# Performance work log

Hardware: AMD Instinct MI355X
Metric: run time of the kernel (lower is better)

## Reference

```python
import math
import jax, jax.numpy as jnp
import numpy as np

B, N, L, E, D = 8, 4096, 256, 64, 128
Q4 = D // 4

def setup_inputs():
    key = jax.random.key(0)
    ks = jax.random.split(key, 24)
    s = 0.05
    return {
        "x_L": jax.random.normal(ks[0], (B, N), jnp.float32),
        "x_y_mask": (jax.random.uniform(ks[1], (B, N)) < 0.7).astype(jnp.float32),
        "y_mask_L": (jax.random.uniform(ks[2], (B, N)) < 0.3).astype(jnp.float32),
        "x_y_mark": jax.random.normal(ks[3], (B, L, 1), jnp.float32),
        "variable_indices": jax.random.randint(ks[4], (B, N), 0, E, jnp.int32),
        "time_indices": jax.random.randint(ks[5], (B, N), 0, L, jnp.int32),
        "N_OBS_MAX": N,
        "W_obs": jax.random.normal(ks[6], (2, D)) * s,
        "b_obs": jnp.zeros((D,), jnp.float32),
        "W_temp": jax.random.normal(ks[7], (1, D)) * s,
        "b_temp": jnp.zeros((D,), jnp.float32),
        "var_he_w": jax.random.normal(ks[8], (E, D), jnp.float32),
        "Wq": jax.random.normal(ks[9], (D, D)) * s,
        "bq": jnp.zeros((D,), jnp.float32),
        "Wk": jax.random.normal(ks[10], (D, D)) * s,
        "bk": jnp.zeros((D,), jnp.float32),
        "Wv": jax.random.normal(ks[11], (D, D)) * s,
        "bv": jnp.zeros((D,), jnp.float32),
        "threshold": jnp.float32(0.0),
        "merge_coef": jnp.float32(0.5),
        "Pr_w": jax.random.normal(ks[12], (3 * D, Q4)) * s,
        "Pr_b": jnp.zeros((Q4,), jnp.float32),
        "Pi_w": jax.random.normal(ks[13], (D, Q4)) * s,
        "Pi_b": jnp.zeros((Q4,), jnp.float32),
        "Pj_w": jax.random.normal(ks[14], (D, Q4)) * s,
        "Pj_b": jnp.zeros((Q4,), jnp.float32),
        "Pk_w": jax.random.normal(ks[15], (D, Q4)) * s,
        "Pk_b": jnp.zeros((Q4,), jnp.float32),
        "Qr": jnp.eye(Q4, dtype=jnp.float32) + jax.random.normal(ks[16], (Q4, Q4)) * s,
        "Qi": jax.random.normal(ks[17], (Q4, Q4)) * s,
        "Qj": jax.random.normal(ks[18], (Q4, Q4)) * s,
        "Qk": jax.random.normal(ks[19], (Q4, Q4)) * s,
        "fusion_bias": jnp.zeros((D,), jnp.float32),
    }

def reference(x_L, x_y_mask, y_mask_L, x_y_mark, variable_indices, time_indices,
              N_OBS_MAX, W_obs, b_obs, W_temp, b_temp, var_he_w,
              Wq, bq, Wk, bk, Wv, bv, threshold, merge_coef,
              Pr_w, Pr_b, Pi_w, Pi_b, Pj_w, Pj_b, Pk_w, Pk_b,
              Qr, Qi, Qj, Qk, fusion_bias):
    dt = x_L.dtype
    # --- HypergraphEncoder ---
    x2 = jnp.stack([x_L, 1.0 - x_y_mask + y_mask_L], axis=-1)          # (B,N,2)
    # temporal incidence: node n belongs to time hyperedge time_indices[n]
    t_inc = (time_indices[:, None, :] == jnp.arange(L)[None, :, None]).astype(dt)
    t_inc = t_inc * x_y_mask[:, None, :]                                # (B,L,N)
    v_inc = (jnp.arange(E)[None, :, None] == variable_indices[:, None, :]).astype(dt)
    v_inc = v_inc * x_y_mask[:, None, :]                                # (B,E,N)
    obs = jax.nn.relu(x2 @ W_obs + b_obs) * x_y_mask[..., None]         # (B,N,D)
    t_he = jnp.sin(x_y_mark @ W_temp + b_temp)                          # (B,L,D)
    v_he = jax.nn.relu(jnp.broadcast_to(var_he_w, (x_L.shape[0], E, D)))  # (B,E,D)
    # --- IrregularityAwareAttention over variable hyperedges ---
    q = v_he @ Wq + bq
    k = v_he @ Wk + bk
    v = v_he @ Wv + bv
    scores = jnp.einsum('bed,bfd->bef', q, k) / math.sqrt(D)            # (B,E,E)
    aux = jnp.einsum('ben,bfn->bef', v_inc, v_inc) / math.sqrt(v_inc.shape[-1])
    m = (aux != 0) & (scores > threshold)
    scores = jnp.where(m, (1.0 - merge_coef) * scores + merge_coef * aux, scores)
    attn = jax.nn.softmax(scores, axis=-1)
    v_he_att = jnp.einsum('bef,bfd->bed', attn, v)                      # (B,E,D)
    # --- gather hyperedge features to nodes via incidence ---
    tg = jnp.einsum('bln,bld->bnd', t_inc, t_he)                        # (B,N,D)
    vg = jnp.einsum('ben,bed->bnd', v_inc, v_he_att)                    # (B,N,D)
    # --- QuaternionStructuredFusion ---
    r = jnp.concatenate([obs, tg, vg], axis=-1) @ Pr_w + Pr_b           # (B,N,D/4)
    i = obs @ Pi_w + Pi_b
    j = tg @ Pj_w + Pj_b
    kq = vg @ Pk_w + Pk_b
    q_in = jnp.concatenate([r, i, j, kq], axis=-1)                      # (B,N,D)
    W = jnp.concatenate([
        jnp.concatenate([Qr, -Qi, -Qj, -Qk], axis=1),
        jnp.concatenate([Qi,  Qr, -Qk,  Qj], axis=1),
        jnp.concatenate([Qj,  Qk,  Qr, -Qi], axis=1),
        jnp.concatenate([Qk, -Qj,  Qi,  Qr], axis=1)], axis=0)          # (D,D)
    return q_in @ W.T + fusion_bias                                     # (B,N,D)
```

## Files before the change

### kernel.cpp

```cpp
#include <hip/hip_runtime.h>
#include <hip/hip_bf16.h>

#define B_ 8
#define N_ 4096
#define L_ 256
#define E_ 64
#define D_ 128

typedef const float* fp;
typedef __attribute__((ext_vector_type(8))) short short8;
typedef __attribute__((ext_vector_type(4))) float f32x4;

__device__ __forceinline__ short f2bf(float x) {
  __hip_bfloat16 h = __float2bfloat16(x);
  return __builtin_bit_cast(short, h);
}

__device__ __constant__ int   selT[16] = {0,1,2,3, 1,0,3,2, 2,3,0,1, 3,2,1,0};
__device__ __constant__ float sgnT[16] = {1.f,-1.f,-1.f,-1.f, 1.f,1.f,-1.f,1.f,
                                          1.f,1.f,1.f,-1.f, 1.f,-1.f,1.f,1.f};


__global__ __launch_bounds__(256) void k_setup(
    fp Pr_w, fp Pi_w, fp Pj_w, fp Pk_w,
    fp Pr_b, fp Pi_b, fp Pj_b, fp Pk_b,
    fp Qr, fp Qi, fp Qj, fp Qk, fp fusion_bias,
    fp var_he_w, fp Wq, fp bq, fp Wk, fp bk, fp Wv, fp bv,
    fp xmask, const int* vidx,
    float* ws) {
  int bid = blockIdx.x, tid = threadIdx.x;
  float* M = ws;
  unsigned short* m0frag = (unsigned short*)ws;
  float* c = ws + 49152;
  float* qkv = ws + 49280;
  float* cnt = ws + 73856;
  if (bid < 96) {
    __shared__ float qlds[4][32][33];
    {
      fp Qsrc[4] = {Qr, Qi, Qj, Qk};
      for (int lid = tid; lid < 4096; lid += 256) {
        int mat = lid >> 10, el = lid & 1023;
        qlds[mat][el >> 5][el & 31] = Qsrc[mat][el];
      }
    }
    __syncthreads();
    int m = bid >> 5, di0 = (bid & 31) * 4;
    int sub = tid >> 7, dd = tid & 127;
    int br = dd >> 5, a = dd & 31;
    const float* w0 = qlds[br][a];
    int t1 = br * 4 + m + 1;
    const float* w1 = qlds[selT[t1]][a];
    float s1 = sgnT[t1];
    fp Pm = (m == 0) ? Pi_w : (m == 1) ? Pj_w : Pk_w;
#pragma unroll
    for (int ii = 0; ii < 2; ++ii) {
      int di = di0 + ii * 2 + sub;
      const float* pr = Pr_w + (m * 128 + di) * 32;
      const float* pm = Pm + di * 32;
      float acc = 0.f;
#pragma unroll
      for (int q = 0; q < 32; ++q)
        acc += pr[q] * w0[q] + s1 * pm[q] * w1[q];
      if (m == 0) {
        int fn = dd >> 4, ft = di >> 5, hi = (di >> 3) & 3, j = di & 7;
        int l = hi * 16 + (dd & 15);
        m0frag[((fn * 4 + ft) * 64 + l) * 8 + j] = (unsigned short)f2bf(acc);
      } else {
        M[m * 16384 + di * 128 + dd] = acc;
      }
    }
    if (bid == 0 && tid < 128) {
      float acc = fusion_bias ? fusion_bias[tid] : 0.f;
#pragma unroll
      for (int bc = 0; bc < 4; ++bc) {
        fp Pb = (bc == 0) ? Pr_b : (bc == 1) ? Pi_b : (bc == 2) ? Pj_b : Pk_b;
        int t = br * 4 + bc;
        const float* wr = qlds[selT[t]][a];
        float sg = sgnT[t];
        float part = 0.f;
#pragma unroll
        for (int q = 0; q < 32; ++q) part += Pb[q] * wr[q];
        acc += sg * part;
      }
      c[tid] = acc;
    }
  } else if (bid < 192) {
    int id = (bid - 96) * 256 + tid;
    int which = id >> 13, rem = id & 8191, e = rem >> 7, d = rem & 127;
    fp W = (which == 0) ? Wq : (which == 1) ? Wk : Wv;
    fp bb = (which == 0) ? bq : (which == 1) ? bk : bv;
    float acc = bb[d];
    for (int d2 = 0; d2 < 128; ++d2)
      acc += fmaxf(var_he_w[e * 128 + d2], 0.f) * W[d2 * 128 + d];
    qkv[id] = acc;
  } else {
    __shared__ int hc[64];
    int b = bid - 192;
    if (tid < 64) hc[tid] = 0;
    __syncthreads();
    for (int n = tid; n < N_; n += 256)
      if (xmask[b * N_ + n] != 0.f)
        atomicAdd(&hc[vidx[b * N_ + n] & 63], 1);
    __syncthreads();
    if (tid < 64) cnt[b * 64 + tid] = (float)hc[tid];
  }
}

__global__ __launch_bounds__(128) void k_mid(
    fp thr_p, fp mc_p, fp mark, fp W_temp, fp b_temp,
    float* ws) {
  const float* M1 = ws + 16384;
  const float* M2 = ws + 32768;
  const float* qkv = ws + 49280;
  const float* cnt = ws + 73856;
  float* VG = ws + 74368;
  float* TG = ws + 139904;
  int bid = blockIdx.x, t = threadIdx.x;
  if (bid < 512) {
    __shared__ float buf[128];
    __shared__ float attn_s[64];
    int b = bid >> 6, e = bid & 63;
    const float* q = qkv;
    const float* k = qkv + 8192;
    const float* v = qkv + 16384;
    int f = t & 63, h = t >> 6;
    float part = 0.f;
    for (int d = h * 64; d < h * 64 + 64; ++d)
      part += q[e * 128 + d] * k[f * 128 + d];
    buf[t] = part;
    __syncthreads();
    if (t < 64) {
      float s = (buf[t] + buf[t + 64]) * 0.08838834764831845f;
      if (t == e) {
        float aux = cnt[b * 64 + e] * (1.f / 64.f);
        float thv = thr_p ? thr_p[0] : 0.f;
        float mc = mc_p ? mc_p[0] : 0.5f;
        if (aux != 0.f && s > thv) s = (1.f - mc) * s + mc * aux;
      }
      float m = s;
      for (int o = 32; o; o >>= 1) m = fmaxf(m, __shfl_xor(m, o));
      float ex = __expf(s - m);
      float sum = ex;
      for (int o = 32; o; o >>= 1) sum += __shfl_xor(sum, o);
      attn_s[t] = ex / sum;
    }
    __syncthreads();
    float va = 0.f;
    for (int ff = 0; ff < 64; ++ff) va += attn_s[ff] * v[ff * 128 + t];
    __syncthreads();
    buf[t] = va;
    __syncthreads();
    float acc = 0.f;
    for (int di = 0; di < 128; ++di) acc += buf[di] * M2[di * 128 + t];
    VG[(b * 64 + e) * 128 + t] = acc;
  } else {
    __shared__ float tb[4][128];
    int r0 = (bid - 512) * 4;
#pragma unroll
    for (int r = 0; r < 4; ++r)
      tb[r][t] = sinf(mark[r0 + r] * W_temp[t] + b_temp[t]);
    __syncthreads();
    float a0 = 0.f, a1 = 0.f, a2 = 0.f, a3 = 0.f;
    for (int di = 0; di < 128; ++di) {
      float m1v = M1[di * 128 + t];
      a0 += tb[0][di] * m1v;
      a1 += tb[1][di] * m1v;
      a2 += tb[2][di] * m1v;
      a3 += tb[3][di] * m1v;
    }
    TG[(r0 + 0) * 128 + t] = a0;
    TG[(r0 + 1) * 128 + t] = a1;
    TG[(r0 + 2) * 128 + t] = a2;
    TG[(r0 + 3) * 128 + t] = a3;
  }
}

__global__ __launch_bounds__(256) void k_mainf(
    fp x_L, fp x_y_mask, fp y_mask_L, const int* vidx, const int* tidx,
    fp W_obs, fp b_obs, const float* ws, float* out) {
  __shared__ short8 m0s[2048];
  const short8* fr = (const short8*)ws;
  const float* c = ws + 49152;
  const float* VG = ws + 74368;
  const float* TG = ws + 139904;
  int tid = threadIdx.x;
#pragma unroll
  for (int i = 0; i < 8; ++i) m0s[tid + i * 256] = fr[tid + i * 256];
  __syncthreads();

  int w = tid >> 6, l = tid & 63;
  int nb = blockIdx.x * 64 + w * 16;
  int b = blockIdx.x >> 6;

  int nodeA = nb + (l & 15);
  float mask = x_y_mask[nodeA];
  float xa = x_L[nodeA];
  float xb = 1.f - mask + y_mask_L[nodeA];
  short8 af[4];
#pragma unroll
  for (int ft = 0; ft < 4; ++ft) {
#pragma unroll
    for (int j = 0; j < 8; ++j) {
      int col = ft * 32 + ((l >> 4) << 3) + j;
      float o = fmaxf(xa * W_obs[col] + xb * W_obs[128 + col] + b_obs[col], 0.f) * mask;
      af[ft][j] = f2bf(o);
    }
  }

  f32x4 acc[8];
#pragma unroll
  for (int fn = 0; fn < 8; ++fn) acc[fn] = (f32x4)(0.f);
#pragma unroll
  for (int fn = 0; fn < 8; ++fn) {
#pragma unroll
    for (int ft = 0; ft < 4; ++ft) {
      short8 bf = m0s[(fn * 4 + ft) * 64 + l];
      acc[fn] = __builtin_amdgcn_mfma_f32_16x16x32_bf16(af[ft], bf, acc[fn], 0, 0, 0);
    }
  }

  int colbase = l & 15;
  float cv[8];
#pragma unroll
  for (int fn = 0; fn < 8; ++fn) cv[fn] = c[fn * 16 + colbase];
#pragma unroll
  for (int rg = 0; rg < 4; ++rg) {
    int node = nb + ((l >> 4) << 2) + rg;
    float m2 = x_y_mask[node];
    int ti = tidx[node] & 255, vi = vidx[node] & 63;
    const float* tgr = TG + (b * 256 + ti) * 128;
    const float* vgr = VG + (b * 64 + vi) * 128;
    float* orow = out + node * 128;
#pragma unroll
    for (int fn = 0; fn < 8; ++fn) {
      int col = fn * 16 + colbase;
      orow[col] = acc[fn][rg] + cv[fn] + m2 * (tgr[col] + vgr[col]);
    }
  }
}

extern "C" void kernel_launch(void* const* d_in, const int* in_sizes, int n_in,
                              void* d_out, int out_size, void* d_ws, size_t ws_size,
                              hipStream_t stream) {
  const void* P[33];
  {
    int p = 0;
    for (int i = 0; i < 33; ++i) {
      bool isopt = (i == 6 || i == 18 || i == 19);
      if (isopt) {
        if (p < n_in && in_sizes[p] == 1) P[i] = d_in[p++];
        else P[i] = nullptr;
      } else {
        P[i] = (p < n_in) ? d_in[p++] : nullptr;
      }
    }
  }
  fp x_L      = (fp)P[0];
  fp x_y_mask = (fp)P[1];
  fp y_mask_L = (fp)P[2];
  fp x_y_mark = (fp)P[3];
  const int* vidx = (const int*)P[4];
  const int* tidx = (const int*)P[5];
  fp W_obs = (fp)P[7];
  fp b_obs = (fp)P[8];
  fp W_temp = (fp)P[9];
  fp b_temp = (fp)P[10];
  fp var_he_w = (fp)P[11];
  fp Wq = (fp)P[12]; fp bq = (fp)P[13];
  fp Wk = (fp)P[14]; fp bk = (fp)P[15];
  fp Wv = (fp)P[16]; fp bv = (fp)P[17];
  fp thr = (fp)P[18]; fp mc = (fp)P[19];
  fp Pr_w = (fp)P[20]; fp Pr_b = (fp)P[21];
  fp Pi_w = (fp)P[22]; fp Pi_b = (fp)P[23];
  fp Pj_w = (fp)P[24]; fp Pj_b = (fp)P[25];
  fp Pk_w = (fp)P[26]; fp Pk_b = (fp)P[27];
  fp Qr = (fp)P[28]; fp Qi = (fp)P[29];
  fp Qj = (fp)P[30]; fp Qk = (fp)P[31];
  fp fusion_bias = (fp)P[32];

  float* ws = (float*)d_ws;

  hipLaunchKernelGGL(k_setup, dim3(200), dim3(256), 0, stream,
                     Pr_w, Pi_w, Pj_w, Pk_w, Pr_b, Pi_b, Pj_b, Pk_b,
                     Qr, Qi, Qj, Qk, fusion_bias,
                     var_he_w, Wq, bq, Wk, bk, Wv, bv,
                     x_y_mask, vidx, ws);
  hipLaunchKernelGGL(k_mid, dim3(1024), dim3(128), 0, stream,
                     thr, mc, x_y_mark, W_temp, b_temp, ws);
  hipLaunchKernelGGL(k_mainf, dim3(512), dim3(256), 0, stream,
                     x_L, x_y_mask, y_mask_L, vidx, tidx, W_obs, b_obs,
                     ws, (float*)d_out);
}
```

Measured before the change: 44.23 us.

## Batch four hyperedges per block in k_mid and store transposed K

The attention part of k_mid now handles four hyperedges per block instead of one. It reads a transposed copy of K written by k_setup so the score loop reads coalesced rows, and it reuses each loaded V and M2 element across four accumulators. The temporal projection part handles eight rows per block instead of four, which cuts the grid from 1024 to 384 blocks. The goal is less redundant global traffic in the mid stage, at the cost of fewer blocks for latency hiding and extra workspace for kT.

New measurement: 44.44 us. Within noise of the previous version (+0.5%).

```diff
diff --git a/kernel.cpp b/kernel.cpp
--- a/kernel.cpp
+++ b/kernel.cpp
@@ -34,6 +34,7 @@
   float* c = ws + 49152;
   float* qkv = ws + 49280;
   float* cnt = ws + 73856;
+  float* kT = ws + 402048;
   if (bid < 96) {
     __shared__ float qlds[4][32][33];
     {
@@ -93,6 +94,7 @@
     for (int d2 = 0; d2 < 128; ++d2)
       acc += fmaxf(var_he_w[e * 128 + d2], 0.f) * W[d2 * 128 + d];
     qkv[id] = acc;
+    if (which == 1) kT[d * 64 + e] = acc;
   } else {
     __shared__ int hc[64];
     int b = bid - 192;
@@ -115,63 +117,77 @@
   const float* cnt = ws + 73856;
   float* VG = ws + 74368;
   float* TG = ws + 139904;
+  const float* kT = ws + 402048;
   int bid = blockIdx.x, t = threadIdx.x;
-  if (bid < 512) {
-    __shared__ float buf[128];
-    __shared__ float attn_s[64];
-    int b = bid >> 6, e = bid & 63;
+  if (bid < 128) {
+    __shared__ float q4[4][128];
+    __shared__ float attn4[4][64];
+    __shared__ float va4[4][128];
+    int b = bid >> 4, e0 = (bid & 15) << 2;
     const float* q = qkv;
-    const float* k = qkv + 8192;
     const float* v = qkv + 16384;
-    int f = t & 63, h = t >> 6;
-    float part = 0.f;
-    for (int d = h * 64; d < h * 64 + 64; ++d)
-      part += q[e * 128 + d] * k[f * 128 + d];
-    buf[t] = part;
-    __syncthreads();
-    if (t < 64) {
-      float s = (buf[t] + buf[t + 64]) * 0.08838834764831845f;
-      if (t == e) {
+    for (int i = t; i < 512; i += 128)
+      q4[i >> 7][i & 127] = q[(e0 + (i >> 7)) * 128 + (i & 127)];
+    __syncthreads();
+    int w = t >> 6, f = t & 63;
+    float thv = thr_p ? thr_p[0] : 0.f;
+    float mcv = mc_p ? mc_p[0] : 0.5f;
+#pragma unroll
+    for (int pass = 0; pass < 2; ++pass) {
+      int ee = pass * 2 + w;
+      int e = e0 + ee;
+      float acc = 0.f;
+      for (int d = 0; d < 128; ++d) acc += q4[ee][d] * kT[d * 64 + f];
+      float s = acc * 0.08838834764831845f;
+      if (f == e) {
         float aux = cnt[b * 64 + e] * (1.f / 64.f);
-        float thv = thr_p ? thr_p[0] : 0.f;
-        float mc = mc_p ? mc_p[0] : 0.5f;
-        if (aux != 0.f && s > thv) s = (1.f - mc) * s + mc * aux;
+        if (aux != 0.f && s > thv) s = (1.f - mcv) * s + mcv * aux;
       }
       float m = s;
       for (int o = 32; o; o >>= 1) m = fmaxf(m, __shfl_xor(m, o));
       float ex = __expf(s - m);
       float sum = ex;
       for (int o = 32; o; o >>= 1) sum += __shfl_xor(sum, o);
-      attn_s[t] = ex / sum;
-    }
-    __syncthreads();
-    float va = 0.f;
-    for (int ff = 0; ff < 64; ++ff) va += attn_s[ff] * v[ff * 128 + t];
-    __syncthreads();
-    buf[t] = va;
-    __syncthreads();
-    float acc = 0.f;
-    for (int di = 0; di < 128; ++di) acc += buf[di] * M2[di * 128 + t];
-    VG[(b * 64 + e) * 128 + t] = acc;
+      attn4[ee][f] = ex / sum;
+    }
+    __syncthreads();
+    float a0 = 0.f, a1 = 0.f, a2 = 0.f, a3 = 0.f;
+    for (int ff = 0; ff < 64; ++ff) {
+      float vv = v[ff * 128 + t];
+      a0 += attn4[0][ff] * vv;
+      a1 += attn4[1][ff] * vv;
+      a2 += attn4[2][ff] * vv;
+      a3 += attn4[3][ff] * vv;
+    }
+    va4[0][t] = a0; va4[1][t] = a1; va4[2][t] = a2; va4[3][t] = a3;
+    __syncthreads();
+    float g0 = 0.f, g1 = 0.f, g2 = 0.f, g3 = 0.f;
+    for (int di = 0; di < 128; ++di) {
+      float m2v = M2[di * 128 + t];
+      g0 += va4[0][di] * m2v;
+      g1 += va4[1][di] * m2v;
+      g2 += va4[2][di] * m2v;
+      g3 += va4[3][di] * m2v;
+    }
+    float* vgb = VG + (b * 64 + e0) * 128 + t;
+    vgb[0] = g0; vgb[128] = g1; vgb[256] = g2; vgb[384] = g3;
   } else {
-    __shared__ float tb[4][128];
-    int r0 = (bid - 512) * 4;
-#pragma unroll
-    for (int r = 0; r < 4; ++r)
+    __shared__ float tb[8][128];
+    int r0 = (bid - 128) * 8;
+#pragma unroll
+    for (int r = 0; r < 8; ++r)
       tb[r][t] = sinf(mark[r0 + r] * W_temp[t] + b_temp[t]);
     __syncthreads();
-    float a0 = 0.f, a1 = 0.f, a2 = 0.f, a3 = 0.f;
+    float a[8];
+#pragma unroll
+    for (int r = 0; r < 8; ++r) a[r] = 0.f;
     for (int di = 0; di < 128; ++di) {
       float m1v = M1[di * 128 + t];
-      a0 += tb[0][di] * m1v;
-      a1 += tb[1][di] * m1v;
-      a2 += tb[2][di] * m1v;
-      a3 += tb[3][di] * m1v;
-    }
-    TG[(r0 + 0) * 128 + t] = a0;
-    TG[(r0 + 1) * 128 + t] = a1;
-    TG[(r0 + 2) * 128 + t] = a2;
-    TG[(r0 + 3) * 128 + t] = a3;
+#pragma unroll
+      for (int r = 0; r < 8; ++r) a[r] += tb[r][di] * m1v;
+    }
+#pragma unroll
+    for (int r = 0; r < 8; ++r) TG[(r0 + r) * 128 + t] = a[r];
   }
 }
 
@@ -285,7 +301,7 @@
                      Qr, Qi, Qj, Qk, fusion_bias,
                      var_he_w, Wq, bq, Wk, bk, Wv, bv,
                      x_y_mask, vidx, ws);
-  hipLaunchKernelGGL(k_mid, dim3(1024), dim3(128), 0, stream,
+  hipLaunchKernelGGL(k_mid, dim3(384), dim3(128), 0, stream,
                      thr, mc, x_y_mark, W_temp, b_temp, ws);
   hipLaunchKernelGGL(k_mainf, dim3(512), dim3(256), 0, stream,
                      x_L, x_y_mask, y_mask_L, vidx, tidx, W_obs, b_obs,
```
